# Optimization experiments

Measured on AMD Instinct MI355X. Metric: run time of the kernel, lower is better.

Reference implementation:

```python
import jax, jax.numpy as jnp
import numpy as np

K = 7          # kernel_size
PAD = 3        # (dilation*(K-1)+1)//2
EPS = 1e-5     # BatchNorm eps
B, CIN, H, W = 4, 256, 56, 56
CR = 32        # rel_planes
COUT = 256     # out_planes
SP = 8         # share_planes
HN = COUT // SP  # attention heads = 32
OFFS = [(dy, dx) for dy in range(K) for dx in range(K)]


def setup_inputs() -> dict:
    key = jax.random.key(0)
    ks = jax.random.split(key, 24)
    def n(i, shape, s=0.05):
        return jax.random.normal(ks[i], shape, dtype=jnp.float32) * s
    def pos(i, shape):  # positive values for BN gamma / running var
        return jax.random.uniform(ks[i], shape, dtype=jnp.float32, minval=0.5, maxval=1.5)
    return {
        "x": jax.random.normal(ks[0], (B, CIN, H, W), dtype=jnp.float32),
        "w1c": n(1, (CR, CIN)),  "b1c": n(2, (CR,)),
        "w2c": n(3, (CR, CIN)),  "b2c": n(4, (CR,)),
        "w3c": n(5, (COUT, CIN)), "b3c": n(6, (COUT,)),
        "bn1_g": pos(7, (CR,)), "bn1_b": n(8, (CR,)), "bn1_m": n(9, (CR,)), "bn1_v": pos(10, (CR,)),
        "cw1": n(11, (CR, CR)),
        "bn2_g": pos(12, (CR,)), "bn2_b": n(13, (CR,)), "bn2_m": n(14, (CR,)), "bn2_v": pos(15, (CR,)),
        "cw2": n(16, (HN, CR)), "cw2_b": n(17, (HN,)),
    }


def _conv1x1(x, w, b):
    # x: [B,C,H,W], w: [O,C]
    return jnp.einsum('bchw,oc->bohw', x, w) + b[None, :, None, None]


def _bn(y, g, b, m, v):
    # inference BatchNorm2d over channel axis 1; y is 4D
    inv = g / jnp.sqrt(v + EPS)
    return y * inv[None, :, None, None] + (b - m * inv)[None, :, None, None]


def reference(x, w1c, b1c, w2c, b2c, w3c, b3c,
              bn1_g, bn1_b, bn1_m, bn1_v, cw1,
              bn2_g, bn2_b, bn2_m, bn2_v, cw2, cw2_b):
    x1 = _conv1x1(x, w1c, b1c)   # [B,CR,H,W]  query
    x2 = _conv1x1(x, w2c, b2c)   # [B,CR,H,W]  key
    x3 = _conv1x1(x, w3c, b3c)   # [B,COUT,H,W] value

    # Subtraction2 with reflection padding (pad_mode=1):
    # diff[b,c,k,i] = x1[b,c,i] - patch_k(x2)[b,c,i]
    x2p = jnp.pad(x2, ((0, 0), (0, 0), (PAD, PAD), (PAD, PAD)), mode='reflect')
    diff = jnp.stack([x1 - x2p[:, :, dy:dy + H, dx:dx + W] for dy, dx in OFFS],
                     axis=2)                      # [B,CR,49,H,W]
    diff = diff.reshape(B, CR, K * K, H * W)      # [B,CR,49,HW]

    # conv_w: BN -> ReLU -> 1x1 conv (no bias) -> BN -> ReLU -> 1x1 conv
    y = jax.nn.relu(_bn(diff, bn1_g, bn1_b, bn1_m, bn1_v))
    y = jnp.einsum('bkln,ok->boln', y, cw1)       # [B,CR,49,HW]
    y = jax.nn.relu(_bn(y, bn2_g, bn2_b, bn2_m, bn2_v))
    logits = jnp.einsum('bkln,ok->boln', y, cw2) + cw2_b[None, :, None, None]
    wgt = jax.nn.softmax(logits, axis=2)          # softmax over k^2, [B,HN,49,HW]
    wgt = wgt.reshape(B, HN, K * K, H, W)

    # Aggregation with reflection padding: out[b,c,i] = sum_k patch_k(x3)[b,c,i] * w[b,c//SP,k,i]
    x3p = jnp.pad(x3, ((0, 0), (0, 0), (PAD, PAD), (PAD, PAD)), mode='reflect')
    out = jnp.zeros((B, HN, SP, H, W), dtype=x.dtype)
    for k, (dy, dx) in enumerate(OFFS):
        patch = x3p[:, :, dy:dy + H, dx:dx + W].reshape(B, HN, SP, H, W)
        out = out + patch * wgt[:, :, k][:, :, None]
    return out.reshape(B, COUT, H, W)
```

## Files before the change

kernel.cpp:

```cpp
#include <hip/hip_runtime.h>
#include <math.h>

#define HW_N   3136
#define W_DIM  56
#define C_IN   256
#define C_R    32
#define C_OUT  256
#define C_ALL  320
#define K2D    49
#define RS     40
#define BN_EPS 1e-5f

typedef _Float16 h2 __attribute__((ext_vector_type(2)));
typedef _Float16 h4 __attribute__((ext_vector_type(4)));
typedef _Float16 h8 __attribute__((ext_vector_type(8)));
typedef __fp16  g2 __attribute__((ext_vector_type(2)));
typedef __fp16  g4 __attribute__((ext_vector_type(4)));
typedef __fp16  g8 __attribute__((ext_vector_type(8)));
typedef float   f4 __attribute__((ext_vector_type(4)));
typedef unsigned int u32;
typedef unsigned int u32x4 __attribute__((ext_vector_type(4)));

__device__ __forceinline__ h2 pkrtz(float a, float b) {
    g2 r = __builtin_amdgcn_cvt_pkrtz(a, b);
    return __builtin_bit_cast(h2, r);
}

__device__ __forceinline__ g8 pack8(float4 a, float4 b) {
    g2 p0 = __builtin_amdgcn_cvt_pkrtz(a.x, a.y);
    g2 p1 = __builtin_amdgcn_cvt_pkrtz(a.z, a.w);
    g2 p2 = __builtin_amdgcn_cvt_pkrtz(b.x, b.y);
    g2 p3 = __builtin_amdgcn_cvt_pkrtz(b.z, b.w);
    g8 o;
    o[0] = p0[0]; o[1] = p0[1]; o[2] = p1[0]; o[3] = p1[1];
    o[4] = p2[0]; o[5] = p2[1]; o[6] = p3[0]; o[7] = p3[1];
    return o;
}

__device__ __forceinline__ int refl(int v) {
    v = (v < 0) ? -v : v;
    return (v > 55) ? (110 - v) : v;
}

__device__ __forceinline__ void wave_fence() {
    asm volatile("s_waitcnt lgkmcnt(0)" ::: "memory");
}

__global__ __launch_bounds__(256) void k_conv_mfma(
    const float* __restrict__ x,
    const float* __restrict__ w1c, const float* __restrict__ w2c,
    const float* __restrict__ w3c,
    const float* __restrict__ b1c, const float* __restrict__ b2c,
    const float* __restrict__ b3c, __fp16* __restrict__ xall16)
{
    __shared__ __align__(16) _Float16 smem[32 * 328];
    const int t = threadIdx.x, w = t >> 6, lane = t & 63;
    const int quad = lane >> 4, l16 = lane & 15;
    const int b = blockIdx.z, pos0 = blockIdx.x * 32;

    {
        const int p = t & 31;
        const int gb = t >> 5;
        const float* xp = x + (size_t)b * C_IN * HW_N + pos0 + p;
#pragma unroll
        for (int i = 0; i < 4; ++i) {
            const int g = i * 8 + gb;
            const int ci = g * 8;
            float v[8];
#pragma unroll
            for (int j = 0; j < 8; ++j) v[j] = xp[(size_t)(ci + j) * HW_N];
            g8 o;
#pragma unroll
            for (int jj = 0; jj < 4; ++jj) {
                const g2 pr = __builtin_amdgcn_cvt_pkrtz(v[2 * jj], v[2 * jj + 1]);
                o[2 * jj] = pr[0]; o[2 * jj + 1] = pr[1];
            }
            *(g8*)((__fp16*)smem + (size_t)(p * 32 + (g ^ (p & 7))) * 8) = o;
        }
    }
    __syncthreads();

    const float* wrow[5]; float bias[5];
#pragma unroll
    for (int nt = 0; nt < 5; ++nt) {
        const int co = w * 80 + nt * 16 + l16;
        wrow[nt] = (co < 32) ? (w1c + co * C_IN)
                 : (co < 64) ? (w2c + (co - 32) * C_IN)
                             : (w3c + (co - 64) * C_IN);
        bias[nt] = (co < 32) ? b1c[co] : (co < 64) ? b2c[co - 32] : b3c[co - 64];
    }

    f4 acc[2][5];
#pragma unroll
    for (int mt = 0; mt < 2; ++mt)
#pragma unroll
        for (int nt = 0; nt < 5; ++nt) acc[mt][nt] = (f4){0.f, 0.f, 0.f, 0.f};

    const int xo = l16 & 7;
#pragma unroll
    for (int ks = 0; ks < 8; ++ks) {
        g8 bf[5];
#pragma unroll
        for (int nt = 0; nt < 5; ++nt) {
            const float* wp = wrow[nt] + ks * 32 + quad * 8;
            bf[nt] = pack8(*(const float4*)wp, *(const float4*)(wp + 4));
        }
#pragma unroll
        for (int mt = 0; mt < 2; ++mt) {
            const int row = mt * 16 + l16;
            const g8 af = *(const g8*)((const __fp16*)smem
                          + (size_t)(row * 32 + ((ks * 4 + quad) ^ xo)) * 8);
#pragma unroll
            for (int nt = 0; nt < 5; ++nt)
                acc[mt][nt] = __builtin_amdgcn_mfma_f32_16x16x32_f16(af, bf[nt], acc[mt][nt], 0, 0, 0);
        }
    }
    __syncthreads();

#pragma unroll
    for (int mt = 0; mt < 2; ++mt)
#pragma unroll
        for (int nt = 0; nt < 5; ++nt) {
            const int co = w * 80 + nt * 16 + l16;
#pragma unroll
            for (int r = 0; r < 4; ++r) {
                const int row = mt * 16 + quad * 4 + r;
                smem[row * 328 + co] = (_Float16)(acc[mt][nt][r] + bias[nt]);
            }
        }
    __syncthreads();
#pragma unroll
    for (int i = 0; i < 5; ++i) {
        const int idx = i * 256 + t;
        const int row = idx / 40, c8 = idx - row * 40;
        const g8 v = *(const g8*)((const __fp16*)smem + row * 328 + c8 * 8);
        *(g8*)(xall16 + ((size_t)b * HW_N + pos0 + row) * C_ALL + c8 * 8) = v;
    }
}

__global__ __launch_bounds__(256) void k_attn(
    const __fp16* __restrict__ xq,
    const float* __restrict__ bn1_g, const float* __restrict__ bn1_b,
    const float* __restrict__ bn1_m, const float* __restrict__ bn1_v,
    const float* __restrict__ cw1,
    const float* __restrict__ bn2_g, const float* __restrict__ bn2_b,
    const float* __restrict__ bn2_m, const float* __restrict__ bn2_v,
    const float* __restrict__ cw2, const float* __restrict__ cw2_b,
    float* __restrict__ out)
{
    __shared__ __align__(16) _Float16 tbuf[4][64 * RS];
    __shared__ int pk[4][52];
    const int tid = threadIdx.x;
    const int w = tid >> 6, lane = tid & 63;
    const int b = blockIdx.y;
    const int bid  = blockIdx.x;
    const int posb = (bid & 7) * 98 + (bid >> 3);
    const int pos0 = posb * 4;
    const int pos  = pos0 + w;
    const int y0 = pos / W_DIM, x0 = pos - y0 * W_DIM;
    const __fp16* __restrict__ base16 = xq + (size_t)b * HW_N * C_ALL;
    _Float16* tb = tbuf[w];
    float* stage_w = (float*)(tb + 49 * RS);
    (void)cw2_b;

    {
        const int c8  = lane & 3;
        const int r16 = lane >> 2;
        const int cb  = c8 * 8;
        float iv[8], bt[8];
        {
            float gg[8], bb_[8], mm[8], vv[8];
            *(float4*)(gg)      = *(const float4*)(bn1_g + cb);
            *(float4*)(gg + 4)  = *(const float4*)(bn1_g + cb + 4);
            *(float4*)(bb_)     = *(const float4*)(bn1_b + cb);
            *(float4*)(bb_ + 4) = *(const float4*)(bn1_b + cb + 4);
            *(float4*)(mm)      = *(const float4*)(bn1_m + cb);
            *(float4*)(mm + 4)  = *(const float4*)(bn1_m + cb + 4);
            *(float4*)(vv)      = *(const float4*)(bn1_v + cb);
            *(float4*)(vv + 4)  = *(const float4*)(bn1_v + cb + 4);
#pragma unroll
            for (int j = 0; j < 8; ++j) {
                iv[j] = gg[j] * rsqrtf(vv[j] + BN_EPS);
                bt[j] = bb_[j] - mm[j] * iv[j];
            }
        }
        const h8 x1v = *(const h8*)(base16 + (size_t)pos * C_ALL + cb);
        float x1f[8];
#pragma unroll
        for (int j = 0; j < 8; ++j) x1f[j] = (float)x1v[j];

        auto bnrow = [&](int k) {
            const int dy = k / 7, dx = k - dy * 7;
            const int rp = refl(y0 + dy - 3) * W_DIM + refl(x0 + dx - 3);
            if (c8 == 0) pk[w][k] = rp;
            const h8 x2v = *(const h8*)(base16 + (size_t)rp * C_ALL + 32 + cb);
            float tv[8];
#pragma unroll
            for (int j = 0; j < 8; ++j)
                tv[j] = fmaxf((x1f[j] - (float)x2v[j]) * iv[j] + bt[j], 0.f);
            g8 o;
#pragma unroll
            for (int q = 0; q < 4; ++q) {
                const g2 pr = __builtin_amdgcn_cvt_pkrtz(tv[2 * q], tv[2 * q + 1]);
                o[2 * q] = pr[0]; o[2 * q + 1] = pr[1];
            }
            *(g8*)((__fp16*)tb + k * RS + cb) = o;
        };
#pragma unroll
        for (int j = 0; j < 3; ++j) bnrow(j * 16 + r16);
        if (r16 == 0) bnrow(48);
    }
    wave_fence();

    const int quad = lane >> 4, l16 = lane & 15;
    f4 acc[4][2];

    {
        g8 bf[2];
#pragma unroll
        for (int nt = 0; nt < 2; ++nt) {
            const float* wr = cw1 + (nt * 16 + l16) * C_R + quad * 8;
            bf[nt] = pack8(*(const float4*)wr, *(const float4*)(wr + 4));
        }
#pragma unroll
        for (int mt = 0; mt < 4; ++mt) {
            acc[mt][0] = (f4){0.f, 0.f, 0.f, 0.f};
            acc[mt][1] = (f4){0.f, 0.f, 0.f, 0.f};
            const g8 af = *(const g8*)((const __fp16*)tb + (mt * 16 + l16) * RS + quad * 8);
            acc[mt][0] = __builtin_amdgcn_mfma_f32_16x16x32_f16(af, bf[0], acc[mt][0], 0, 0, 0);
            acc[mt][1] = __builtin_amdgcn_mfma_f32_16x16x32_f16(af, bf[1], acc[mt][1], 0, 0, 0);
        }
    }
    wave_fence();

#pragma unroll
    for (int nt = 0; nt < 2; ++nt) {
        const int o = nt * 16 + l16;
        const float iv = bn2_g[o] * rsqrtf(bn2_v[o] + BN_EPS);
        const float bt = bn2_b[o] - bn2_m[o] * iv;
#pragma unroll
        for (int mt = 0; mt < 4; ++mt)
#pragma unroll
            for (int r = 0; r < 4; ++r) {
                const int row = mt * 16 + quad * 4 + r;
                tb[row * RS + o] = (_Float16)fmaxf(acc[mt][nt][r] * iv + bt, 0.f);
            }
    }
    wave_fence();

    {
        g8 bf[2];
#pragma unroll
        for (int nt = 0; nt < 2; ++nt) {
            const float* wr = cw2 + (nt * 16 + l16) * C_R + quad * 8;
            bf[nt] = pack8(*(const float4*)wr, *(const float4*)(wr + 4));
        }
#pragma unroll
        for (int mt = 0; mt < 4; ++mt) {
            acc[mt][0] = (f4){0.f, 0.f, 0.f, 0.f};
            acc[mt][1] = (f4){0.f, 0.f, 0.f, 0.f};
            const g8 af = *(const g8*)((const __fp16*)tb + (mt * 16 + l16) * RS + quad * 8);
            acc[mt][0] = __builtin_amdgcn_mfma_f32_16x16x32_f16(af, bf[0], acc[mt][0], 0, 0, 0);
            acc[mt][1] = __builtin_amdgcn_mfma_f32_16x16x32_f16(af, bf[1], acc[mt][1], 0, 0, 0);
        }
    }
    wave_fence();

#pragma unroll
    for (int nt = 0; nt < 2; ++nt) {
        float s = 0.f;
#pragma unroll
        for (int mt = 0; mt < 4; ++mt)
#pragma unroll
            for (int r = 0; r < 4; ++r) {
                const int k = mt * 16 + quad * 4 + r;
                const float e = (k < K2D) ? __expf(acc[mt][nt][r]) : 0.f;
                acc[mt][nt][r] = e;
                s += e;
            }
        s += __shfl_xor(s, 16, 64);
        s += __shfl_xor(s, 32, 64);
        const float rs = 1.f / s;
        const int o = nt * 16 + l16;
#pragma unroll
        for (int mt = 0; mt < 4; ++mt)
#pragma unroll
            for (int r = 0; r < 4; ++r) {
                const int row = mt * 16 + quad * 4 + r;
                if (row < K2D)
                    tb[row * RS + o] = (_Float16)(acc[mt][nt][r] * rs);
            }
    }
    wave_fence();

    {
        const int hn = lane & 31;
        const int hf = lane >> 5;
        const __fp16* vb = base16 + 64 + hn * 8;
        float a0 = 0.f, a1 = 0.f, a2 = 0.f, a3 = 0.f;
        float a4 = 0.f, a5 = 0.f, a6 = 0.f, a7 = 0.f;
#pragma unroll 6
        for (int i = 0; i < 24; ++i) {
            const int k = 2 * i + hf;
            const int rp = pk[w][k];
            const float wv = (float)tb[k * RS + hn];
            const h8 v = *(const h8*)(vb + (size_t)rp * C_ALL);
            a0 = fmaf((float)v[0], wv, a0);
            a1 = fmaf((float)v[1], wv, a1);
            a2 = fmaf((float)v[2], wv, a2);
            a3 = fmaf((float)v[3], wv, a3);
            a4 = fmaf((float)v[4], wv, a4);
            a5 = fmaf((float)v[5], wv, a5);
            a6 = fmaf((float)v[6], wv, a6);
            a7 = fmaf((float)v[7], wv, a7);
        }
        if (hf == 0) {
            const int rp = pk[w][48];
            const float wv = (float)tb[48 * RS + hn];
            const h8 v = *(const h8*)(vb + (size_t)rp * C_ALL);
            a0 = fmaf((float)v[0], wv, a0);
            a1 = fmaf((float)v[1], wv, a1);
            a2 = fmaf((float)v[2], wv, a2);
            a3 = fmaf((float)v[3], wv, a3);
            a4 = fmaf((float)v[4], wv, a4);
            a5 = fmaf((float)v[5], wv, a5);
            a6 = fmaf((float)v[6], wv, a6);
            a7 = fmaf((float)v[7], wv, a7);
        }
        a0 += __shfl_xor(a0, 32, 64);
        a1 += __shfl_xor(a1, 32, 64);
        a2 += __shfl_xor(a2, 32, 64);
        a3 += __shfl_xor(a3, 32, 64);
        a4 += __shfl_xor(a4, 32, 64);
        a5 += __shfl_xor(a5, 32, 64);
        a6 += __shfl_xor(a6, 32, 64);
        a7 += __shfl_xor(a7, 32, 64);
        if (hf == 0) {
            f4 o0 = {a0, a1, a2, a3};
            f4 o1 = {a4, a5, a6, a7};
            *(f4*)&stage_w[hn * 8]     = o0;
            *(f4*)&stage_w[hn * 8 + 4] = o1;
        }
    }
    __syncthreads();

    {
        const int c = tid;
        const float* st0 = (const float*)(tbuf[0] + 49 * RS);
        const float* st1 = (const float*)(tbuf[1] + 49 * RS);
        const float* st2 = (const float*)(tbuf[2] + 49 * RS);
        const float* st3 = (const float*)(tbuf[3] + 49 * RS);
        float4 o;
        o.x = st0[c]; o.y = st1[c];
        o.z = st2[c]; o.w = st3[c];
        *(float4*)(out + ((size_t)b * C_OUT + c) * HW_N + pos0) = o;
    }
}

extern "C" void kernel_launch(void* const* d_in, const int* in_sizes, int n_in,
                              void* d_out, int out_size, void* d_ws, size_t ws_size,
                              hipStream_t stream)
{
    const float* x     = (const float*)d_in[0];
    const float* w1c   = (const float*)d_in[1];
    const float* b1c   = (const float*)d_in[2];
    const float* w2c   = (const float*)d_in[3];
    const float* b2c   = (const float*)d_in[4];
    const float* w3c   = (const float*)d_in[5];
    const float* b3c   = (const float*)d_in[6];
    const float* bn1_g = (const float*)d_in[7];
    const float* bn1_b = (const float*)d_in[8];
    const float* bn1_m = (const float*)d_in[9];
    const float* bn1_v = (const float*)d_in[10];
    const float* cw1   = (const float*)d_in[11];
    const float* bn2_g = (const float*)d_in[12];
    const float* bn2_b = (const float*)d_in[13];
    const float* bn2_m = (const float*)d_in[14];
    const float* bn2_v = (const float*)d_in[15];
    const float* cw2   = (const float*)d_in[16];
    const float* cw2_b = (const float*)d_in[17];

    __fp16* xall16 = (__fp16*)d_ws;

    k_conv_mfma<<<dim3(98, 1, 4), 256, 0, stream>>>(x, w1c, w2c, w3c,
                                                    b1c, b2c, b3c, xall16);
    k_attn<<<dim3(784, 4, 1), 256, 0, stream>>>(xall16,
        bn1_g, bn1_b, bn1_m, bn1_v, cw1,
        bn2_g, bn2_b, bn2_m, bn2_v, cw2, cw2_b, (float*)d_out);
}
```

Measured before the change: 153.4 us.

## Halve conv tile, hoist attention weights, prefetch value rows, fuse BN1 algebra

After: 171.7 us. 1.12x slower.

```diff
diff --git a/kernel.cpp b/kernel.cpp
--- a/kernel.cpp
+++ b/kernel.cpp
@@ -53,18 +53,18 @@
     const float* __restrict__ b1c, const float* __restrict__ b2c,
     const float* __restrict__ b3c, __fp16* __restrict__ xall16)
 {
-    __shared__ __align__(16) _Float16 smem[32 * 328];
+    __shared__ __align__(16) _Float16 smem[16 * 328];
     const int t = threadIdx.x, w = t >> 6, lane = t & 63;
     const int quad = lane >> 4, l16 = lane & 15;
-    const int b = blockIdx.z, pos0 = blockIdx.x * 32;
+    const int b = blockIdx.z, pos0 = blockIdx.x * 16;
 
     {
-        const int p = t & 31;
-        const int gb = t >> 5;
+        const int p  = t & 15;
+        const int gb = t >> 4;
         const float* xp = x + (size_t)b * C_IN * HW_N + pos0 + p;
 #pragma unroll
-        for (int i = 0; i < 4; ++i) {
-            const int g = i * 8 + gb;
+        for (int i = 0; i < 2; ++i) {
+            const int g = i * 16 + gb;
             const int ci = g * 8;
             float v[8];
 #pragma unroll
@@ -90,11 +90,9 @@
         bias[nt] = (co < 32) ? b1c[co] : (co < 64) ? b2c[co - 32] : b3c[co - 64];
     }
 
-    f4 acc[2][5];
-#pragma unroll
-    for (int mt = 0; mt < 2; ++mt)
-#pragma unroll
-        for (int nt = 0; nt < 5; ++nt) acc[mt][nt] = (f4){0.f, 0.f, 0.f, 0.f};
+    f4 acc[5];
+#pragma unroll
+    for (int nt = 0; nt < 5; ++nt) acc[nt] = (f4){0.f, 0.f, 0.f, 0.f};
 
     const int xo = l16 & 7;
 #pragma unroll
@@ -105,36 +103,32 @@
             const float* wp = wrow[nt] + ks * 32 + quad * 8;
             bf[nt] = pack8(*(const float4*)wp, *(const float4*)(wp + 4));
         }
-#pragma unroll
-        for (int mt = 0; mt < 2; ++mt) {
-            const int row = mt * 16 + l16;
-            const g8 af = *(const g8*)((const __fp16*)smem
-                          + (size_t)(row * 32 + ((ks * 4 + quad) ^ xo)) * 8);
-#pragma unroll
-            for (int nt = 0; nt < 5; ++nt)
-                acc[mt][nt] = __builtin_amdgcn_mfma_f32_16x16x32_f16(af, bf[nt], acc[mt][nt], 0, 0, 0);
-        }
+        const g8 af = *(const g8*)((const __fp16*)smem
+                      + (size_t)(l16 * 32 + ((ks * 4 + quad) ^ xo)) * 8);
+#pragma unroll
+        for (int nt = 0; nt < 5; ++nt)
+            acc[nt] = __builtin_amdgcn_mfma_f32_16x16x32_f16(af, bf[nt], acc[nt], 0, 0, 0);
     }
     __syncthreads();
 
 #pragma unroll
-    for (int mt = 0; mt < 2; ++mt)
-#pragma unroll
-        for (int nt = 0; nt < 5; ++nt) {
-            const int co = w * 80 + nt * 16 + l16;
-#pragma unroll
-            for (int r = 0; r < 4; ++r) {
-                const int row = mt * 16 + quad * 4 + r;
-                smem[row * 328 + co] = (_Float16)(acc[mt][nt][r] + bias[nt]);
-            }
-        }
+    for (int nt = 0; nt < 5; ++nt) {
+        const int co = w * 80 + nt * 16 + l16;
+#pragma unroll
+        for (int r = 0; r < 4; ++r) {
+            const int row = quad * 4 + r;
+            smem[row * 328 + co] = (_Float16)(acc[nt][r] + bias[nt]);
+        }
+    }
     __syncthreads();
 #pragma unroll
-    for (int i = 0; i < 5; ++i) {
+    for (int i = 0; i < 3; ++i) {
         const int idx = i * 256 + t;
-        const int row = idx / 40, c8 = idx - row * 40;
-        const g8 v = *(const g8*)((const __fp16*)smem + row * 328 + c8 * 8);
-        *(g8*)(xall16 + ((size_t)b * HW_N + pos0 + row) * C_ALL + c8 * 8) = v;
+        if (idx < 640) {
+            const int row = idx / 40, c8 = idx - row * 40;
+            const g8 v = *(const g8*)((const __fp16*)smem + row * 328 + c8 * 8);
+            *(g8*)(xall16 + ((size_t)b * HW_N + pos0 + row) * C_ALL + c8 * 8) = v;
+        }
     }
 }
 
@@ -163,11 +157,26 @@
     float* stage_w = (float*)(tb + 49 * RS);
     (void)cw2_b;
 
+    const int quad = lane >> 4, l16 = lane & 15;
+
+    g8 bf1[2], bf2[2];
+    float iv2c[2], bt2c[2];
+#pragma unroll
+    for (int nt = 0; nt < 2; ++nt) {
+        const float* wr1 = cw1 + (nt * 16 + l16) * C_R + quad * 8;
+        bf1[nt] = pack8(*(const float4*)wr1, *(const float4*)(wr1 + 4));
+        const float* wr2 = cw2 + (nt * 16 + l16) * C_R + quad * 8;
+        bf2[nt] = pack8(*(const float4*)wr2, *(const float4*)(wr2 + 4));
+        const int o = nt * 16 + l16;
+        iv2c[nt] = bn2_g[o] * rsqrtf(bn2_v[o] + BN_EPS);
+        bt2c[nt] = bn2_b[o] - bn2_m[o] * iv2c[nt];
+    }
+
     {
         const int c8  = lane & 3;
         const int r16 = lane >> 2;
         const int cb  = c8 * 8;
-        float iv[8], bt[8];
+        float niv[8], a1[8];
         {
             float gg[8], bb_[8], mm[8], vv[8];
             *(float4*)(gg)      = *(const float4*)(bn1_g + cb);
@@ -178,16 +187,16 @@
             *(float4*)(mm + 4)  = *(const float4*)(bn1_m + cb + 4);
             *(float4*)(vv)      = *(const float4*)(bn1_v + cb);
             *(float4*)(vv + 4)  = *(const float4*)(bn1_v + cb + 4);
+            const h8 x1v = *(const h8*)(base16 + (size_t)pos * C_ALL + cb);
 #pragma unroll
             for (int j = 0; j < 8; ++j) {
-                iv[j] = gg[j] * rsqrtf(vv[j] + BN_EPS);
-                bt[j] = bb_[j] - mm[j] * iv[j];
+                const float iv = gg[j] * rsqrtf(vv[j] + BN_EPS);
+                const float bt = bb_[j] - mm[j] * iv;
+                a1[j]  = fmaf((float)x1v[j], iv, bt);
+                niv[j] = -iv;
             }
         }
-        const h8 x1v = *(const h8*)(base16 + (size_t)pos * C_ALL + cb);
-        float x1f[8];
-#pragma unroll
-        for (int j = 0; j < 8; ++j) x1f[j] = (float)x1v[j];
+        const h2 hz = {};
 
         auto bnrow = [&](int k) {
             const int dy = k / 7, dx = k - dy * 7;
@@ -197,14 +206,19 @@
             float tv[8];
 #pragma unroll
             for (int j = 0; j < 8; ++j)
-                tv[j] = fmaxf((x1f[j] - (float)x2v[j]) * iv[j] + bt[j], 0.f);
-            g8 o;
-#pragma unroll
-            for (int q = 0; q < 4; ++q) {
-                const g2 pr = __builtin_amdgcn_cvt_pkrtz(tv[2 * q], tv[2 * q + 1]);
-                o[2 * q] = pr[0]; o[2 * q + 1] = pr[1];
-            }
-            *(g8*)((__fp16*)tb + k * RS + cb) = o;
+                tv[j] = fmaf((float)x2v[j], niv[j], a1[j]);
+            h2 p0 = pkrtz(tv[0], tv[1]), p1 = pkrtz(tv[2], tv[3]);
+            h2 p2 = pkrtz(tv[4], tv[5]), p3 = pkrtz(tv[6], tv[7]);
+            p0 = __builtin_elementwise_max(p0, hz);
+            p1 = __builtin_elementwise_max(p1, hz);
+            p2 = __builtin_elementwise_max(p2, hz);
+            p3 = __builtin_elementwise_max(p3, hz);
+            u32x4 o;
+            o[0] = __builtin_bit_cast(u32, p0);
+            o[1] = __builtin_bit_cast(u32, p1);
+            o[2] = __builtin_bit_cast(u32, p2);
+            o[3] = __builtin_bit_cast(u32, p3);
+            *(u32x4*)&tb[k * RS + cb] = o;
         };
 #pragma unroll
         for (int j = 0; j < 3; ++j) bnrow(j * 16 + r16);
@@ -212,32 +226,30 @@
     }
     wave_fence();
 
-    const int quad = lane >> 4, l16 = lane & 15;
+    const int hn5 = lane & 31;
+    const int hf5 = lane >> 5;
+    const __fp16* vb5 = base16 + 64 + hn5 * 8;
+    h8 pre[12];
+#pragma unroll
+    for (int i = 0; i < 12; ++i)
+        pre[i] = *(const h8*)(vb5 + (size_t)pk[w][2 * i + hf5] * C_ALL);
+
     f4 acc[4][2];
 
-    {
-        g8 bf[2];
-#pragma unroll
-        for (int nt = 0; nt < 2; ++nt) {
-            const float* wr = cw1 + (nt * 16 + l16) * C_R + quad * 8;
-            bf[nt] = pack8(*(const float4*)wr, *(const float4*)(wr + 4));
-        }
-#pragma unroll
-        for (int mt = 0; mt < 4; ++mt) {
-            acc[mt][0] = (f4){0.f, 0.f, 0.f, 0.f};
-            acc[mt][1] = (f4){0.f, 0.f, 0.f, 0.f};
-            const g8 af = *(const g8*)((const __fp16*)tb + (mt * 16 + l16) * RS + quad * 8);
-            acc[mt][0] = __builtin_amdgcn_mfma_f32_16x16x32_f16(af, bf[0], acc[mt][0], 0, 0, 0);
-            acc[mt][1] = __builtin_amdgcn_mfma_f32_16x16x32_f16(af, bf[1], acc[mt][1], 0, 0, 0);
-        }
+#pragma unroll
+    for (int mt = 0; mt < 4; ++mt) {
+        acc[mt][0] = (f4){0.f, 0.f, 0.f, 0.f};
+        acc[mt][1] = (f4){0.f, 0.f, 0.f, 0.f};
+        const g8 af = *(const g8*)((const __fp16*)tb + (mt * 16 + l16) * RS + quad * 8);
+        acc[mt][0] = __builtin_amdgcn_mfma_f32_16x16x32_f16(af, bf1[0], acc[mt][0], 0, 0, 0);
+        acc[mt][1] = __builtin_amdgcn_mfma_f32_16x16x32_f16(af, bf1[1], acc[mt][1], 0, 0, 0);
     }
     wave_fence();
 
 #pragma unroll
     for (int nt = 0; nt < 2; ++nt) {
         const int o = nt * 16 + l16;
-        const float iv = bn2_g[o] * rsqrtf(bn2_v[o] + BN_EPS);
-        const float bt = bn2_b[o] - bn2_m[o] * iv;
+        const float iv = iv2c[nt], bt = bt2c[nt];
 #pragma unroll
         for (int mt = 0; mt < 4; ++mt)
 #pragma unroll
@@ -248,21 +260,13 @@
     }
     wave_fence();
 
-    {
-        g8 bf[2];
-#pragma unroll
-        for (int nt = 0; nt < 2; ++nt) {
-            const float* wr = cw2 + (nt * 16 + l16) * C_R + quad * 8;
-            bf[nt] = pack8(*(const float4*)wr, *(const float4*)(wr + 4));
-        }
-#pragma unroll
-        for (int mt = 0; mt < 4; ++mt) {
-            acc[mt][0] = (f4){0.f, 0.f, 0.f, 0.f};
-            acc[mt][1] = (f4){0.f, 0.f, 0.f, 0.f};
-            const g8 af = *(const g8*)((const __fp16*)tb + (mt * 16 + l16) * RS + quad * 8);
-            acc[mt][0] = __builtin_amdgcn_mfma_f32_16x16x32_f16(af, bf[0], acc[mt][0], 0, 0, 0);
-            acc[mt][1] = __builtin_amdgcn_mfma_f32_16x16x32_f16(af, bf[1], acc[mt][1], 0, 0, 0);
-        }
+#pragma unroll
+    for (int mt = 0; mt < 4; ++mt) {
+        acc[mt][0] = (f4){0.f, 0.f, 0.f, 0.f};
+        acc[mt][1] = (f4){0.f, 0.f, 0.f, 0.f};
+        const g8 af = *(const g8*)((const __fp16*)tb + (mt * 16 + l16) * RS + quad * 8);
+        acc[mt][0] = __builtin_amdgcn_mfma_f32_16x16x32_f16(af, bf2[0], acc[mt][0], 0, 0, 0);
+        acc[mt][1] = __builtin_amdgcn_mfma_f32_16x16x32_f16(af, bf2[1], acc[mt][1], 0, 0, 0);
     }
     wave_fence();
 
@@ -294,17 +298,13 @@
     wave_fence();
 
     {
-        const int hn = lane & 31;
-        const int hf = lane >> 5;
-        const __fp16* vb = base16 + 64 + hn * 8;
         float a0 = 0.f, a1 = 0.f, a2 = 0.f, a3 = 0.f;
         float a4 = 0.f, a5 = 0.f, a6 = 0.f, a7 = 0.f;
-#pragma unroll 6
-        for (int i = 0; i < 24; ++i) {
-            const int k = 2 * i + hf;
-            const int rp = pk[w][k];
-            const float wv = (float)tb[k * RS + hn];
-            const h8 v = *(const h8*)(vb + (size_t)rp * C_ALL);
+#pragma unroll
+        for (int i = 0; i < 12; ++i) {
+            const int k = 2 * i + hf5;
+            const float wv = (float)tb[k * RS + hn5];
+            const h8 v = pre[i];
             a0 = fmaf((float)v[0], wv, a0);
             a1 = fmaf((float)v[1], wv, a1);
             a2 = fmaf((float)v[2], wv, a2);
@@ -314,10 +314,12 @@
             a6 = fmaf((float)v[6], wv, a6);
             a7 = fmaf((float)v[7], wv, a7);
         }
-        if (hf == 0) {
-            const int rp = pk[w][48];
-            const float wv = (float)tb[48 * RS + hn];
-            const h8 v = *(const h8*)(vb + (size_t)rp * C_ALL);
+#pragma unroll 6
+        for (int i = 12; i < 24; ++i) {
+            const int k = 2 * i + hf5;
+            const int rp = pk[w][k];
+            const float wv = (float)tb[k * RS + hn5];
+            const h8 v = *(const h8*)(vb5 + (size_t)rp * C_ALL);
             a0 = fmaf((float)v[0], wv, a0);
             a1 = fmaf((float)v[1], wv, a1);
             a2 = fmaf((float)v[2], wv, a2);
@@ -327,6 +329,19 @@
             a6 = fmaf((float)v[6], wv, a6);
             a7 = fmaf((float)v[7], wv, a7);
         }
+        if (hf5 == 0) {
+            const int rp = pk[w][48];
+            const float wv = (float)tb[48 * RS + hn5];
+            const h8 v = *(const h8*)(vb5 + (size_t)rp * C_ALL);
+            a0 = fmaf((float)v[0], wv, a0);
+            a1 = fmaf((float)v[1], wv, a1);
+            a2 = fmaf((float)v[2], wv, a2);
+            a3 = fmaf((float)v[3], wv, a3);
+            a4 = fmaf((float)v[4], wv, a4);
+            a5 = fmaf((float)v[5], wv, a5);
+            a6 = fmaf((float)v[6], wv, a6);
+            a7 = fmaf((float)v[7], wv, a7);
+        }
         a0 += __shfl_xor(a0, 32, 64);
         a1 += __shfl_xor(a1, 32, 64);
         a2 += __shfl_xor(a2, 32, 64);
@@ -335,11 +350,11 @@
         a5 += __shfl_xor(a5, 32, 64);
         a6 += __shfl_xor(a6, 32, 64);
         a7 += __shfl_xor(a7, 32, 64);
-        if (hf == 0) {
+        if (hf5 == 0) {
             f4 o0 = {a0, a1, a2, a3};
             f4 o1 = {a4, a5, a6, a7};
-            *(f4*)&stage_w[hn * 8]     = o0;
-            *(f4*)&stage_w[hn * 8 + 4] = o1;
+            *(f4*)&stage_w[hn5 * 8]     = o0;
+            *(f4*)&stage_w[hn5 * 8 + 4] = o1;
         }
     }
     __syncthreads();
@@ -382,8 +397,8 @@
 
     __fp16* xall16 = (__fp16*)d_ws;
 
-    k_conv_mfma<<<dim3(98, 1, 4), 256, 0, stream>>>(x, w1c, w2c, w3c,
-                                                    b1c, b2c, b3c, xall16);
+    k_conv_mfma<<<dim3(196, 1, 4), 256, 0, stream>>>(x, w1c, w2c, w3c,
+                                                     b1c, b2c, b3c, xall16);
     k_attn<<<dim3(784, 4, 1), 256, 0, stream>>>(xall16,
         bn1_g, bn1_b, bn1_m, bn1_v, cw1,
         bn2_g, bn2_b, bn2_m, bn2_v, cw2, cw2_b, (float*)d_out);
```
